# Optimization experiments

Measured on AMD Instinct MI355X. Metric: run time of the kernel, lower is better.

## Reference

```python
import jax, jax.numpy as jnp
import numpy as np
from jax import lax

HID = 896          # hidden_size
HALF = HID // 2    # 448
BINS = 256         # 2 ** (bits/2), bits=16
B, T = 16, 2048


def setup_inputs() -> dict:
    key = jax.random.key(0)
    ks = jax.random.split(key, 16)
    rn = lambda k, shape, s: (jax.random.normal(k, shape, jnp.float32) * s)
    inp = {
        'conditional': jax.random.normal(ks[0], (B, T, 3, HID), jnp.float32),
        'input_signal': jax.random.randint(ks[1], (B, T, 2), 0, BINS, jnp.int32),
        'target_coarse': jax.random.randint(ks[2], (B, T, 1), 0, BINS, jnp.int32),
        # project_coarse_input: Linear(2, 3*half, bias=False)
        'Wc': rn(ks[3], (2, 3 * HALF), 0.5),
        # project_fine_input: Linear(3, 3*half, bias=False)
        'Wf': rn(ks[4], (3, 3 * HALF), 0.5),
        # stripped GRU hidden-to-hidden weights/biases (input projection is rnn_input itself)
        'W_hh': rn(ks[5], (HID, 3 * HID), 0.02),
        'b_ih': jnp.zeros((3 * HID,), jnp.float32),
        'b_hh': jnp.zeros((3 * HID,), jnp.float32),
        # to_bins_coarse: Linear(half, half) + ReLU + Linear(half, bins)
        'W1c': rn(ks[6], (HALF, HALF), 0.05), 'b1c': jnp.zeros((HALF,), jnp.float32),
        'W2c': rn(ks[7], (HALF, BINS), 0.05), 'b2c': jnp.zeros((BINS,), jnp.float32),
        # to_bins_fine
        'W1f': rn(ks[8], (HALF, HALF), 0.05), 'b1f': jnp.zeros((HALF,), jnp.float32),
        'W2f': rn(ks[9], (HALF, BINS), 0.05), 'b2f': jnp.zeros((BINS,), jnp.float32),
    }
    return inp


def _scale(x):
    # [0, BINS-1] -> [-1, 1]
    return x.astype(jnp.float32) / ((BINS - 1) / 2.0) - 1.0


def reference(conditional, input_signal, target_coarse, Wc, Wf, W_hh, b_ih, b_hh,
              W1c, b1c, W2c, b2c, W1f, b1f, W2f, b2f):
    sig = _scale(input_signal)          # [B, T, 2]
    tc = _scale(target_coarse)          # [B, T, 1]

    coarse_proj = (sig @ Wc).reshape(B, T, 3, HALF)
    fine_proj = (jnp.concatenate([sig, tc], axis=2) @ Wf).reshape(B, T, 3, HALF)
    # concat along feature halves -> [B, T, 3, HID], add conditional, flatten gates
    rnn_input = jnp.concatenate([coarse_proj, fine_proj], axis=3) + conditional
    rnn_input = rnn_input.reshape(B, T, 3 * HID) + b_ih
    xs = rnn_input.transpose(1, 0, 2)   # [T, B, 3*HID]

    def step(h, x_t):
        gh = h @ W_hh + b_hh                      # [B, 3*HID]
        xr, xz, xn = jnp.split(x_t, 3, axis=-1)
        hr, hz, hn = jnp.split(gh, 3, axis=-1)
        r = jax.nn.sigmoid(xr + hr)
        z = jax.nn.sigmoid(xz + hz)
        n = jnp.tanh(xn + r * hn)
        h_new = (1.0 - z) * n + z * h
        return h_new, h_new

    h0 = jnp.zeros((B, HID), jnp.float32)
    last_hidden, hidden_states = lax.scan(step, h0, xs)   # [T, B, HID]
    hidden_states = hidden_states.transpose(1, 0, 2)      # [B, T, HID]

    hidden_coarse = hidden_states[..., :HALF]
    # NOTE: original code applies to_bins_fine to hidden_coarse as well (faithful).
    out_coarse = jax.nn.relu(hidden_coarse @ W1c + b1c) @ W2c + b2c
    out_fine = jax.nn.relu(hidden_coarse @ W1f + b1f) @ W2f + b2f
    return out_coarse, out_fine, last_hidden
```

## Files before the change

kernel.cpp:

```cpp
#include <hip/hip_runtime.h>
#include <hip/hip_cooperative_groups.h>

namespace cg = cooperative_groups;

#define BB 16
#define TT 2048
#define HIDN 896
#define HALFN 448
#define NBINS 256
#define NWG 112
#define NTHR 64
#define WSTR 904

typedef __attribute__((ext_vector_type(8))) short short8;
typedef __attribute__((ext_vector_type(4))) float f32x4;
typedef __attribute__((ext_vector_type(2))) unsigned long long ull2;

__device__ __forceinline__ unsigned short f2bf(float x) {
    unsigned int u = __float_as_uint(x);
    unsigned int r = u + 0x7FFFu + ((u >> 16) & 1u);
    return (unsigned short)(r >> 16);
}

__global__ __launch_bounds__(NTHR, 1)
void scan_kernel(const float* __restrict__ cond,
                 const int*   __restrict__ sig,
                 const int*   __restrict__ tcrs,
                 const float* __restrict__ Wc,
                 const float* __restrict__ Wf,
                 const float* __restrict__ Whh,
                 const float* __restrict__ b_ih,
                 const float* __restrict__ b_hh,
                 unsigned long long* __restrict__ hx,
                 int* __restrict__ slots,
                 unsigned short* __restrict__ hc_out,
                 float* __restrict__ lasth)
{
    __shared__ unsigned short sW[32 * WSTR];

    const int tid  = threadIdx.x;
    const int wg   = blockIdx.x;
    const int cb   = (wg & 7) * 14 + (wg >> 3);
    const int col0 = cb * 8;

    for (int idx = tid; idx < 32 * HIDN; idx += NTHR) {
        int j2 = idx & 31, k = idx >> 5;
        unsigned short wv = 0;
        if (j2 < 16)
            wv = f2bf(Whh[(size_t)k * 2688 + (j2 >> 3) * HIDN + col0 + (j2 & 7)]);
        else if (j2 < 24)
            wv = f2bf(Whh[(size_t)k * 2688 + 2 * HIDN + col0 + (j2 & 7)]);
        sW[j2 * WSTR + k] = wv;
    }
    if (tid == 0)
        __hip_atomic_store(&slots[wg * 16], 0, __ATOMIC_RELAXED, __HIP_MEMORY_SCOPE_AGENT);

    const int l  = tid;
    const int q  = l & 15;
    const int hi = l >> 4;
    const int gA   = q >> 3;
    const int colA = col0 + (q & 7);

    float wpA0, wpA1, wpA2, wpB0, wpB1, wpB2;
    if (colA < HALFN) {
        wpA0 = Wc[gA * HALFN + colA];
        wpA1 = Wc[1344 + gA * HALFN + colA];
        wpA2 = 0.f;
        wpB0 = Wc[2 * HALFN + colA];
        wpB1 = Wc[1344 + 2 * HALFN + colA];
        wpB2 = 0.f;
    } else {
        int ck = colA - HALFN;
        wpA0 = Wf[gA * HALFN + ck];
        wpA1 = Wf[1344 + gA * HALFN + ck];
        wpA2 = Wf[2688 + gA * HALFN + ck];
        wpB0 = Wf[2 * HALFN + ck];
        wpB1 = Wf[1344 + 2 * HALFN + ck];
        wpB2 = Wf[2688 + 2 * HALFN + ck];
    }
    const float biA = b_ih[gA * HIDN + colA];
    const float bhA = b_hh[gA * HIDN + colA];
    const float biB = b_ih[2 * HIDN + colA];
    const float bhB = b_hh[2 * HIDN + colA];

    float hp[4] = {0.f, 0.f, 0.f, 0.f};

    float xcA[4], xcB[4];
    int   si0[4], si1[4], si2[4];

#define PREFETCH(tt) {                                                         \
    int tn_ = (tt) < TT ? (tt) : TT - 1;                                       \
    _Pragma("unroll")                                                          \
    for (int r_ = 0; r_ < 4; ++r_) {                                           \
        size_t bt_ = (size_t)(hi * 4 + r_) * TT + tn_;                         \
        xcA[r_] = cond[(bt_ * 3 + gA) * HIDN + colA];                          \
        xcB[r_] = cond[(bt_ * 3 + 2) * HIDN + colA];                           \
        si0[r_] = sig[bt_ * 2 + 0];                                            \
        si1[r_] = sig[bt_ * 2 + 1];                                            \
        si2[r_] = tcrs[bt_];                                                   \
    } }

    PREFETCH(0);

    __syncthreads();
    cg::this_grid().sync();

    const float inv = 1.f / 127.5f;
    const int zsrc = (l & 48) | 8 | (q & 7);

#define WAITALL(t) { bool ok_;                                                 \
    for (;;) {                                                                 \
        int a_ = __hip_atomic_load(&slots[l * 16],                             \
            __ATOMIC_RELAXED, __HIP_MEMORY_SCOPE_AGENT);                       \
        int b_ = (l < 48) ? __hip_atomic_load(&slots[(l + 64) * 16],           \
            __ATOMIC_RELAXED, __HIP_MEMORY_SCOPE_AGENT) : a_;                  \
        ok_ = (a_ >= (t)) & (b_ >= (t));                                       \
        if (__all(ok_)) break;                                                 \
        __builtin_amdgcn_s_sleep(1);                                           \
    }                                                                          \
    asm volatile("" ::: "memory"); }

#define LOADH(s, V) _Pragma("unroll")                                          \
    for (int i_ = 0; i_ < 7; ++i_) {                                           \
        _Pragma("unroll")                                                      \
        for (int h_ = 0; h_ < 2; ++h_)                                         \
            V[2*i_ + h_] = __hip_atomic_load(                                  \
                &hb[(size_t)(4 * ((s)*7 + i_) + hi) * 32 + h_ * 16 + q],       \
                __ATOMIC_RELAXED, __HIP_MEMORY_SCOPE_AGENT);                   \
    }

#define MFMAS(s, V) _Pragma("unroll")                                          \
    for (int i_ = 0; i_ < 7; ++i_) {                                           \
        ull2 tv_; tv_.x = V[2*i_]; tv_.y = V[2*i_ + 1];                        \
        short8 av_ = __builtin_bit_cast(short8, tv_);                          \
        int ks_ = (s)*7 + i_;                                                  \
        short8 b1_ = *(const short8*)&sW[q * WSTR + hi * 8 + ks_ * 32];        \
        chA[ks_ & 3] = __builtin_amdgcn_mfma_f32_16x16x32_bf16(                \
            av_, b1_, chA[ks_ & 3], 0, 0, 0);                                  \
        short8 b2_ = *(const short8*)&sW[(16 + q) * WSTR + hi * 8 + ks_ * 32]; \
        chB[ks_ & 3] = __builtin_amdgcn_mfma_f32_16x16x32_bf16(                \
            av_, b2_, chB[ks_ & 3], 0, 0, 0);                                  \
    }

    for (int t = 0; t < TT; ++t) {
        f32x4 chA[4] = {}, chB[4] = {};
        if (t > 0) {
            WAITALL(t);
            const unsigned long long* hb = hx + (size_t)(t & 1) * 3584;
            unsigned long long va[14], vb[14];
            LOADH(0, va);
            LOADH(1, vb);
            MFMAS(0, va);
            LOADH(2, va);
            MFMAS(1, vb);
            LOADH(3, vb);
            MFMAS(2, va);
            MFMAS(3, vb);
        }
        f32x4 aA = (chA[0] + chA[1]) + (chA[2] + chA[3]);
        f32x4 aB = (chB[0] + chB[1]) + (chB[2] + chB[3]);

        float xvB[4], sigA[4];
        #pragma unroll
        for (int r = 0; r < 4; ++r) {
            float g0 = (float)si0[r] * inv - 1.f;
            float g1 = (float)si1[r] * inv - 1.f;
            float g2 = (float)si2[r] * inv - 1.f;
            float xvA = xcA[r] + biA + g0*wpA0 + g1*wpA1 + g2*wpA2;
            xvB[r]    = xcB[r] + biB + g0*wpB0 + g1*wpB1 + g2*wpB2;
            sigA[r] = 1.f / (1.f + __expf(-(xvA + aA[r] + bhA)));
        }
        float hnv[4];
        unsigned short hbits[4] = {0, 0, 0, 0};
        #pragma unroll
        for (int r = 0; r < 4; ++r) {
            float zz = __shfl(sigA[r], zsrc);
            float a2v = xvB[r] + sigA[r] * (aB[r] + bhB);
            float e = __expf(-2.f * a2v);
            float n = (1.f - e) / (1.f + e);
            float hn = (1.f - zz) * n + zz * hp[r];
            hnv[r] = hn;
            if (q < 8) { hp[r] = hn; hbits[r] = f2bf(hn); }
        }
        if (t == TT - 1 && q < 8) {
            #pragma unroll
            for (int r = 0; r < 4; ++r)
                lasth[(size_t)(hi * 4 + r) * HIDN + colA] = hnv[r];
        }

        unsigned p32[4];
        unsigned long long hv64[4];
        #pragma unroll
        for (int r = 0; r < 4; ++r) {
            int o1 = __shfl_xor((int)(unsigned)hbits[r], 1);
            p32[r] = ((unsigned)hbits[r] & 0xffffu) | ((unsigned)o1 << 16);
            int o2 = __shfl_xor((int)p32[r], 2);
            hv64[r] = (unsigned long long)p32[r] |
                      ((unsigned long long)(unsigned)o2 << 32);
        }
        if (t < TT - 1 && (q == 0 || q == 4)) {
            unsigned long long* hd = hx + (size_t)((t + 1) & 1) * 3584;
            #pragma unroll
            for (int r = 0; r < 4; ++r)
                __hip_atomic_store(&hd[(size_t)cb * 32 + (q >> 2) * 16 + hi * 4 + r],
                                   hv64[r], __ATOMIC_RELAXED, __HIP_MEMORY_SCOPE_AGENT);
        }
        asm volatile("s_waitcnt vmcnt(0)" ::: "memory");
        if (tid == 0)
            __hip_atomic_store(&slots[wg * 16], t + 1,
                               __ATOMIC_RELAXED, __HIP_MEMORY_SCOPE_AGENT);

        PREFETCH(t + 1);
        if (cb < 56 && q < 8 && !(q & 1)) {
            unsigned* hc32 = (unsigned*)hc_out;
            #pragma unroll
            for (int r = 0; r < 4; ++r)
                hc32[((size_t)(hi * 4 + r) * TT + t) * 224 + cb * 4 + (q >> 1)] = p32[r];
        }
    }
#undef WAITALL
#undef LOADH
#undef MFMAS
#undef PREFETCH
}

template<int RELU_BF16>
__global__ __launch_bounds__(256)
void head_gemm(const unsigned short* __restrict__ A,
               const float* __restrict__ Bw,
               const float* __restrict__ bias,
               unsigned short* __restrict__ Cb,
               float* __restrict__ Cf,
               int N)
{
    const int K = 448;
    __shared__ unsigned short sA[128 * 40];
    __shared__ unsigned short sBt[64 * 40];
    const int tid = threadIdx.x;
    const int w   = tid >> 6;
    const int l   = tid & 63;
    const int wm  = (w >> 1) * 64;
    const int wn  = (w & 1) * 32;
    const int bm  = blockIdx.x * 128;
    const int bn  = blockIdx.y * 64;

    f32x4 acc[4][2] = {};

    for (int k0 = 0; k0 < K; k0 += 32) {
        #pragma unroll
        for (int it = 0; it < 2; ++it) {
            int idx = tid + it * 256;
            int row = idx >> 2;
            int ck  = (idx & 3) * 8;
            *(float4*)&sA[row * 40 + ck] =
                *(const float4*)(A + (size_t)(bm + row) * K + k0 + ck);
        }
        #pragma unroll
        for (int it = 0; it < 2; ++it) {
            int idx = tid + it * 256;
            int kk = idx >> 4;
            int c4 = (idx & 15) * 4;
            float4 v = *(const float4*)(Bw + (size_t)(k0 + kk) * N + bn + c4);
            sBt[(c4 + 0) * 40 + kk] = f2bf(v.x);
            sBt[(c4 + 1) * 40 + kk] = f2bf(v.y);
            sBt[(c4 + 2) * 40 + kk] = f2bf(v.z);
            sBt[(c4 + 3) * 40 + kk] = f2bf(v.w);
        }
        __syncthreads();
        const int kq = (l >> 4) * 8;
        short8 bv0 = *(const short8*)&sBt[(wn + (l & 15)) * 40 + kq];
        short8 bv1 = *(const short8*)&sBt[(wn + 16 + (l & 15)) * 40 + kq];
        #pragma unroll
        for (int rb = 0; rb < 4; ++rb) {
            short8 av = *(const short8*)&sA[(wm + rb * 16 + (l & 15)) * 40 + kq];
            acc[rb][0] = __builtin_amdgcn_mfma_f32_16x16x32_bf16(av, bv0, acc[rb][0], 0, 0, 0);
            acc[rb][1] = __builtin_amdgcn_mfma_f32_16x16x32_bf16(av, bv1, acc[rb][1], 0, 0, 0);
        }
        __syncthreads();
    }

    #pragma unroll
    for (int rb = 0; rb < 4; ++rb) {
        #pragma unroll
        for (int cbk = 0; cbk < 2; ++cbk) {
            int col = bn + wn + cbk * 16 + (l & 15);
            float bv = bias[col];
            #pragma unroll
            for (int j = 0; j < 4; ++j) {
                int row = bm + wm + rb * 16 + (l >> 4) * 4 + j;
                float v = acc[rb][cbk][j] + bv;
                if (RELU_BF16)
                    Cb[(size_t)row * N + col] = f2bf(fmaxf(v, 0.f));
                else
                    Cf[(size_t)row * N + col] = v;
            }
        }
    }
}

extern "C" void kernel_launch(void* const* d_in, const int* in_sizes, int n_in,
                              void* d_out, int out_size, void* d_ws, size_t ws_size,
                              hipStream_t stream)
{
    const float* cond = (const float*)d_in[0];
    const int*   sig  = (const int*)d_in[1];
    const int*   tcrs = (const int*)d_in[2];
    const float* Wc   = (const float*)d_in[3];
    const float* Wf   = (const float*)d_in[4];
    const float* Whh  = (const float*)d_in[5];
    const float* bih  = (const float*)d_in[6];
    const float* bhh  = (const float*)d_in[7];
    const float* W1c  = (const float*)d_in[8];
    const float* b1c  = (const float*)d_in[9];
    const float* W2c  = (const float*)d_in[10];
    const float* b2c  = (const float*)d_in[11];
    const float* W1f  = (const float*)d_in[12];
    const float* b1f  = (const float*)d_in[13];
    const float* W2f  = (const float*)d_in[14];
    const float* b2f  = (const float*)d_in[15];

    char* ws = (char*)d_ws;
    int* slots               = (int*)ws;
    unsigned long long* hx   = (unsigned long long*)(ws + 8192);
    unsigned short* hc       = (unsigned short*)(ws + 65536);
    unsigned short* hid1     = (unsigned short*)(ws + 65536 + 29360128);

    float* outc  = (float*)d_out;
    float* outf  = outc + (size_t)BB * TT * NBINS;
    float* lasth = outc + 2 * (size_t)BB * TT * NBINS;

    void* args[] = {(void*)&cond, (void*)&sig, (void*)&tcrs, (void*)&Wc, (void*)&Wf,
                    (void*)&Whh, (void*)&bih, (void*)&bhh,
                    (void*)&hx, (void*)&slots, (void*)&hc, (void*)&lasth};
    hipLaunchCooperativeKernel((void*)scan_kernel, dim3(NWG), dim3(NTHR),
                               args, 0, stream);

    dim3 blk(256);
    head_gemm<1><<<dim3(256, 7), blk, 0, stream>>>(hc,   W1c, b1c, hid1, nullptr, 448);
    head_gemm<0><<<dim3(256, 4), blk, 0, stream>>>(hid1, W2c, b2c, nullptr, outc, 256);
    head_gemm<1><<<dim3(256, 7), blk, 0, stream>>>(hc,   W1f, b1f, hid1, nullptr, 448);
    head_gemm<0><<<dim3(256, 4), blk, 0, stream>>>(hid1, W2f, b2f, nullptr, outf, 256);
}
```

Before: 7.708 ms.

## Halve scan workgroups to 56, each computing all three gates for 16 columns

The recurrent scan is repartitioned from 112 single-wave workgroups (8 columns each, with the z gate passed between lanes by shuffle) to 56 workgroups of 16 columns. Each computes the r, z and n gate MFMAs itself, which removes the cross-lane shuffle and halves the number of flags polled at each step's grid barrier. Workgroups launch 256 threads so the bf16 weight staging into LDS is spread over more threads, then the extra waves exit and only one wave runs the scan. The cost is more MFMA and gate work per wave on the serial critical path.

Result: faster. 7.522 ms (-2.4%).

```diff
diff --git a/kernel.cpp b/kernel.cpp
--- a/kernel.cpp
+++ b/kernel.cpp
@@ -8,8 +8,8 @@
 #define HIDN 896
 #define HALFN 448
 #define NBINS 256
-#define NWG 112
-#define NTHR 64
+#define NWG 56
+#define NTHR 256
 #define WSTR 904
 
 typedef __attribute__((ext_vector_type(8))) short short8;
@@ -36,56 +36,50 @@
                  unsigned short* __restrict__ hc_out,
                  float* __restrict__ lasth)
 {
-    __shared__ unsigned short sW[32 * WSTR];
+    __shared__ unsigned short sW[48 * WSTR];
 
     const int tid  = threadIdx.x;
     const int wg   = blockIdx.x;
-    const int cb   = (wg & 7) * 14 + (wg >> 3);
-    const int col0 = cb * 8;
-
-    for (int idx = tid; idx < 32 * HIDN; idx += NTHR) {
-        int j2 = idx & 31, k = idx >> 5;
-        unsigned short wv = 0;
-        if (j2 < 16)
-            wv = f2bf(Whh[(size_t)k * 2688 + (j2 >> 3) * HIDN + col0 + (j2 & 7)]);
-        else if (j2 < 24)
-            wv = f2bf(Whh[(size_t)k * 2688 + 2 * HIDN + col0 + (j2 & 7)]);
-        sW[j2 * WSTR + k] = wv;
+    const int cb   = (wg & 7) * 7 + (wg >> 3);
+    const int col0 = cb * 16;
+
+    for (int idx = tid; idx < 48 * HIDN; idx += NTHR) {
+        int j2 = idx % 48, k = idx / 48;
+        int g = j2 >> 4, c = j2 & 15;
+        sW[j2 * WSTR + k] =
+            f2bf(Whh[(size_t)k * 2688 + g * HIDN + col0 + c]);
     }
     if (tid == 0)
         __hip_atomic_store(&slots[wg * 16], 0, __ATOMIC_RELAXED, __HIP_MEMORY_SCOPE_AGENT);
+
+    __syncthreads();
+    cg::this_grid().sync();
+    if (tid >= 64) return;
 
     const int l  = tid;
     const int q  = l & 15;
     const int hi = l >> 4;
-    const int gA   = q >> 3;
-    const int colA = col0 + (q & 7);
-
-    float wpA0, wpA1, wpA2, wpB0, wpB1, wpB2;
-    if (colA < HALFN) {
-        wpA0 = Wc[gA * HALFN + colA];
-        wpA1 = Wc[1344 + gA * HALFN + colA];
-        wpA2 = 0.f;
-        wpB0 = Wc[2 * HALFN + colA];
-        wpB1 = Wc[1344 + 2 * HALFN + colA];
-        wpB2 = 0.f;
-    } else {
-        int ck = colA - HALFN;
-        wpA0 = Wf[gA * HALFN + ck];
-        wpA1 = Wf[1344 + gA * HALFN + ck];
-        wpA2 = Wf[2688 + gA * HALFN + ck];
-        wpB0 = Wf[2 * HALFN + ck];
-        wpB1 = Wf[1344 + 2 * HALFN + ck];
-        wpB2 = Wf[2688 + 2 * HALFN + ck];
-    }
-    const float biA = b_ih[gA * HIDN + colA];
-    const float bhA = b_hh[gA * HIDN + colA];
-    const float biB = b_ih[2 * HIDN + colA];
-    const float bhB = b_hh[2 * HIDN + colA];
-
+    const int col = col0 + q;
+
+    float wp[3][3], bi[3], bh[3];
+    #pragma unroll
+    for (int g = 0; g < 3; ++g) {
+        if (col < HALFN) {
+            wp[g][0] = Wc[g * HALFN + col];
+            wp[g][1] = Wc[1344 + g * HALFN + col];
+            wp[g][2] = 0.f;
+        } else {
+            int ck = col - HALFN;
+            wp[g][0] = Wf[g * HALFN + ck];
+            wp[g][1] = Wf[1344 + g * HALFN + ck];
+            wp[g][2] = Wf[2688 + g * HALFN + ck];
+        }
+        bi[g] = b_ih[g * HIDN + col];
+        bh[g] = b_hh[g * HIDN + col];
+    }
     float hp[4] = {0.f, 0.f, 0.f, 0.f};
 
-    float xcA[4], xcB[4];
+    float xc[3][4];
     int   si0[4], si1[4], si2[4];
 
 #define PREFETCH(tt) {                                                         \
@@ -93,8 +87,9 @@
     _Pragma("unroll")                                                          \
     for (int r_ = 0; r_ < 4; ++r_) {                                           \
         size_t bt_ = (size_t)(hi * 4 + r_) * TT + tn_;                         \
-        xcA[r_] = cond[(bt_ * 3 + gA) * HIDN + colA];                          \
-        xcB[r_] = cond[(bt_ * 3 + 2) * HIDN + colA];                           \
+        xc[0][r_] = cond[(bt_ * 3 + 0) * HIDN + col];                          \
+        xc[1][r_] = cond[(bt_ * 3 + 1) * HIDN + col];                          \
+        xc[2][r_] = cond[(bt_ * 3 + 2) * HIDN + col];                          \
         si0[r_] = sig[bt_ * 2 + 0];                                            \
         si1[r_] = sig[bt_ * 2 + 1];                                            \
         si2[r_] = tcrs[bt_];                                                   \
@@ -102,19 +97,13 @@
 
     PREFETCH(0);
 
-    __syncthreads();
-    cg::this_grid().sync();
-
     const float inv = 1.f / 127.5f;
-    const int zsrc = (l & 48) | 8 | (q & 7);
 
 #define WAITALL(t) { bool ok_;                                                 \
     for (;;) {                                                                 \
-        int a_ = __hip_atomic_load(&slots[l * 16],                             \
-            __ATOMIC_RELAXED, __HIP_MEMORY_SCOPE_AGENT);                       \
-        int b_ = (l < 48) ? __hip_atomic_load(&slots[(l + 64) * 16],           \
-            __ATOMIC_RELAXED, __HIP_MEMORY_SCOPE_AGENT) : a_;                  \
-        ok_ = (a_ >= (t)) & (b_ >= (t));                                       \
+        int a_ = (l < NWG) ? __hip_atomic_load(&slots[l * 16],                 \
+            __ATOMIC_RELAXED, __HIP_MEMORY_SCOPE_AGENT) : (t);                 \
+        ok_ = (a_ >= (t));                                                     \
         if (__all(ok_)) break;                                                 \
         __builtin_amdgcn_s_sleep(1);                                           \
     }                                                                          \
@@ -125,7 +114,7 @@
         _Pragma("unroll")                                                      \
         for (int h_ = 0; h_ < 2; ++h_)                                         \
             V[2*i_ + h_] = __hip_atomic_load(                                  \
-                &hb[(size_t)(4 * ((s)*7 + i_) + hi) * 32 + h_ * 16 + q],       \
+                &hb[(size_t)(8 * ((s)*7 + i_) + 2 * hi + h_) * 16 + q],        \
                 __ATOMIC_RELAXED, __HIP_MEMORY_SCOPE_AGENT);                   \
     }
 
@@ -133,17 +122,20 @@
     for (int i_ = 0; i_ < 7; ++i_) {                                           \
         ull2 tv_; tv_.x = V[2*i_]; tv_.y = V[2*i_ + 1];                        \
         short8 av_ = __builtin_bit_cast(short8, tv_);                          \
-        int ks_ = (s)*7 + i_;                                                  \
-        short8 b1_ = *(const short8*)&sW[q * WSTR + hi * 8 + ks_ * 32];        \
-        chA[ks_ & 3] = __builtin_amdgcn_mfma_f32_16x16x32_bf16(                \
-            av_, b1_, chA[ks_ & 3], 0, 0, 0);                                  \
-        short8 b2_ = *(const short8*)&sW[(16 + q) * WSTR + hi * 8 + ks_ * 32]; \
-        chB[ks_ & 3] = __builtin_amdgcn_mfma_f32_16x16x32_bf16(                \
-            av_, b2_, chB[ks_ & 3], 0, 0, 0);                                  \
+        int ko_ = ((s)*7 + i_) * 32 + hi * 8;                                  \
+        short8 bR_ = *(const short8*)&sW[q * WSTR + ko_];                      \
+        ch[0][i_ & 1] = __builtin_amdgcn_mfma_f32_16x16x32_bf16(               \
+            av_, bR_, ch[0][i_ & 1], 0, 0, 0);                                 \
+        short8 bZ_ = *(const short8*)&sW[(16 + q) * WSTR + ko_];               \
+        ch[1][i_ & 1] = __builtin_amdgcn_mfma_f32_16x16x32_bf16(               \
+            av_, bZ_, ch[1][i_ & 1], 0, 0, 0);                                 \
+        short8 bN_ = *(const short8*)&sW[(32 + q) * WSTR + ko_];               \
+        ch[2][i_ & 1] = __builtin_amdgcn_mfma_f32_16x16x32_bf16(               \
+            av_, bN_, ch[2][i_ & 1], 0, 0, 0);                                 \
     }
 
     for (int t = 0; t < TT; ++t) {
-        f32x4 chA[4] = {}, chB[4] = {};
+        f32x4 ch[3][2] = {};
         if (t > 0) {
             WAITALL(t);
             const unsigned long long* hb = hx + (size_t)(t & 1) * 3584;
@@ -157,35 +149,34 @@
             MFMAS(2, va);
             MFMAS(3, vb);
         }
-        f32x4 aA = (chA[0] + chA[1]) + (chA[2] + chA[3]);
-        f32x4 aB = (chB[0] + chB[1]) + (chB[2] + chB[3]);
-
-        float xvB[4], sigA[4];
+        f32x4 aR = ch[0][0] + ch[0][1];
+        f32x4 aZ = ch[1][0] + ch[1][1];
+        f32x4 aN = ch[2][0] + ch[2][1];
+
+        float hnv[4];
+        unsigned short hbits[4];
         #pragma unroll
         for (int r = 0; r < 4; ++r) {
             float g0 = (float)si0[r] * inv - 1.f;
             float g1 = (float)si1[r] * inv - 1.f;
             float g2 = (float)si2[r] * inv - 1.f;
-            float xvA = xcA[r] + biA + g0*wpA0 + g1*wpA1 + g2*wpA2;
-            xvB[r]    = xcB[r] + biB + g0*wpB0 + g1*wpB1 + g2*wpB2;
-            sigA[r] = 1.f / (1.f + __expf(-(xvA + aA[r] + bhA)));
-        }
-        float hnv[4];
-        unsigned short hbits[4] = {0, 0, 0, 0};
-        #pragma unroll
-        for (int r = 0; r < 4; ++r) {
-            float zz = __shfl(sigA[r], zsrc);
-            float a2v = xvB[r] + sigA[r] * (aB[r] + bhB);
+            float xvR = xc[0][r] + bi[0] + g0*wp[0][0] + g1*wp[0][1] + g2*wp[0][2];
+            float xvZ = xc[1][r] + bi[1] + g0*wp[1][0] + g1*wp[1][1] + g2*wp[1][2];
+            float xvN = xc[2][r] + bi[2] + g0*wp[2][0] + g1*wp[2][1] + g2*wp[2][2];
+            float sR = 1.f / (1.f + __expf(-(xvR + aR[r] + bh[0])));
+            float sZ = 1.f / (1.f + __expf(-(xvZ + aZ[r] + bh[1])));
+            float a2v = xvN + sR * (aN[r] + bh[2]);
             float e = __expf(-2.f * a2v);
             float n = (1.f - e) / (1.f + e);
-            float hn = (1.f - zz) * n + zz * hp[r];
+            float hn = (1.f - sZ) * n + sZ * hp[r];
+            hp[r] = hn;
             hnv[r] = hn;
-            if (q < 8) { hp[r] = hn; hbits[r] = f2bf(hn); }
-        }
-        if (t == TT - 1 && q < 8) {
+            hbits[r] = f2bf(hn);
+        }
+        if (t == TT - 1) {
             #pragma unroll
             for (int r = 0; r < 4; ++r)
-                lasth[(size_t)(hi * 4 + r) * HIDN + colA] = hnv[r];
+                lasth[(size_t)(hi * 4 + r) * HIDN + col] = hnv[r];
         }
 
         unsigned p32[4];
@@ -198,11 +189,11 @@
             hv64[r] = (unsigned long long)p32[r] |
                       ((unsigned long long)(unsigned)o2 << 32);
         }
-        if (t < TT - 1 && (q == 0 || q == 4)) {
+        if (t < TT - 1 && (q & 3) == 0) {
             unsigned long long* hd = hx + (size_t)((t + 1) & 1) * 3584;
             #pragma unroll
             for (int r = 0; r < 4; ++r)
-                __hip_atomic_store(&hd[(size_t)cb * 32 + (q >> 2) * 16 + hi * 4 + r],
+                __hip_atomic_store(&hd[(size_t)(4 * cb + (q >> 2)) * 16 + hi * 4 + r],
                                    hv64[r], __ATOMIC_RELAXED, __HIP_MEMORY_SCOPE_AGENT);
         }
         asm volatile("s_waitcnt vmcnt(0)" ::: "memory");
@@ -211,11 +202,11 @@
                                __ATOMIC_RELAXED, __HIP_MEMORY_SCOPE_AGENT);
 
         PREFETCH(t + 1);
-        if (cb < 56 && q < 8 && !(q & 1)) {
+        if (cb < 28 && !(q & 1)) {
             unsigned* hc32 = (unsigned*)hc_out;
             #pragma unroll
             for (int r = 0; r < 4; ++r)
-                hc32[((size_t)(hi * 4 + r) * TT + t) * 224 + cb * 4 + (q >> 1)] = p32[r];
+                hc32[((size_t)(hi * 4 + r) * TT + t) * 224 + cb * 8 + (q >> 1)] = p32[r];
         }
     }
 #undef WAITALL
@@ -283,16 +274,16 @@
     for (int rb = 0; rb < 4; ++rb) {
         #pragma unroll
         for (int cbk = 0; cbk < 2; ++cbk) {
-            int col = bn + wn + cbk * 16 + (l & 15);
-            float bv = bias[col];
+            int colo = bn + wn + cbk * 16 + (l & 15);
+            float bv = bias[colo];
             #pragma unroll
             for (int j = 0; j < 4; ++j) {
                 int row = bm + wm + rb * 16 + (l >> 4) * 4 + j;
                 float v = acc[rb][cbk][j] + bv;
                 if (RELU_BF16)
-                    Cb[(size_t)row * N + col] = f2bf(fmaxf(v, 0.f));
+                    Cb[(size_t)row * N + colo] = f2bf(fmaxf(v, 0.f));
                 else
-                    Cf[(size_t)row * N + col] = v;
+                    Cf[(size_t)row * N + colo] = v;
             }
         }
     }
```
